# Optimization experiments

Hardware: AMD Instinct MI355X
Metric: run time of the kernel (lower is better)

Reference implementation:

```python
import jax, jax.numpy as jnp
import numpy as np

B, C, H, W = 8, 16, 64, 64
D, N = 1, 512  # embedding_dim, num_embeddings


def setup_inputs() -> dict:
    key = jax.random.key(0)
    k1, k2 = jax.random.split(key)
    x = jax.random.normal(k1, (B, C, H, W), dtype=jnp.float32)
    weight = jax.random.uniform(k2, (D, N), dtype=jnp.float32)  # torch.rand init
    return {"x": x, "weight": weight}


def reference(x, weight):
    b, c, h, w = x.shape
    # dist: [B,C,H,W,N] via broadcast (D==1), argmin over codebook axis
    dist = (x[..., None] - weight) ** 2
    argmin = jnp.argmin(dist, axis=-1)  # [B,C,H,W] int
    # faithful replication of index_select + view([B,H,W,C]) + permute(0,3,1,2)
    codes = jnp.take(weight.T, argmin.reshape(-1), axis=0)  # [B*C*H*W, 1]
    quantized = codes.reshape(b, h, w, c).transpose(0, 3, 1, 2)  # [B,C,H,W]
    e_latent_loss = jnp.mean((x - jax.lax.stop_gradient(quantized)) ** 2)
    q_latent_loss = jnp.mean((quantized - jax.lax.stop_gradient(x)) ** 2)
    # straight-through estimator
    quantized_st = x + jax.lax.stop_gradient(quantized - x)
    return quantized_st, q_latent_loss, e_latent_loss
```

## Files before the change

kernel.cpp:

```cpp
#include <hip/hip_runtime.h>
#include <hip/hip_bf16.h>


#define E_TOTAL 524288
#define NCODE   512
#define BLOCK   256
#define M       2
#define NBLOCKS_M (E_TOTAL / (BLOCK * M))

#define SKEW(a) ((a) + ((a) >> 5))

__global__ __launch_bounds__(64) void vq_prep_kernel(
    const float* __restrict__ wt, float* __restrict__ sorted) {
  __shared__ float4 lw4[NCODE / 4];
  const int t = threadIdx.x;
  lw4[t] = ((const float4*)wt)[t];
  lw4[t + 64] = ((const float4*)wt)[t + 64];
  __syncthreads();

  const int i = blockIdx.x * 64 + t;
  const float v = ((const float*)lw4)[i];
  int r = 0;
#pragma unroll 8
  for (int j = 0; j < NCODE / 4; ++j) {
    const float4 u = lw4[j];
    const int n0 = 4 * j;
    r += (u.x < v || (u.x == v && (n0 + 0) < i)) ? 1 : 0;
    r += (u.y < v || (u.y == v && (n0 + 1) < i)) ? 1 : 0;
    r += (u.z < v || (u.z == v && (n0 + 2) < i)) ? 1 : 0;
    r += (u.w < v || (u.w == v && (n0 + 3) < i)) ? 1 : 0;
  }
  sorted[r] = v;
}

__global__ __launch_bounds__(BLOCK) void vq_main_kernel(
    const float* __restrict__ x, const float* __restrict__ sorted,
    float* __restrict__ out, double* __restrict__ partial) {
  __shared__ float ls[SKEW(NCODE + 1) + 1];
  __shared__ double lsum[BLOCK / 64];

  const int t = threadIdx.x;
  const int tid = blockIdx.x * BLOCK + t;
  const int o0 = tid * M;
  const int w = o0 & 63;
  const int h = (o0 >> 6) & 63;
  const int c = (o0 >> 12) & 15;
  const int b = o0 >> 16;
  const int ip0 = b * 65536 + h * 1024 + w * 16 + c;

  const float g0 = x[ip0];
  const float g1 = x[ip0 + 16];
  const float2 xo = ((const float2*)x)[tid];

  for (int k = t; k < NCODE; k += BLOCK) ls[SKEW(k + 1)] = sorted[k];
  if (t == 0) ls[SKEW(0)] = -3.0e38f;
  __syncthreads();

  unsigned i0 = 0, i1 = 0;
#pragma unroll
  for (unsigned step = NCODE / 2; step; step >>= 1) {
    const float s0 = ls[SKEW(i0 + step)];
    const float s1 = ls[SKEW(i1 + step)];
    i0 = (s0 <= g0) ? i0 + step : i0;
    i1 = (s1 <= g1) ? i1 + step : i1;
  }
  const float l0 = ls[SKEW(i0)], r0 = ls[SKEW(i0 + 1)];
  const float l1 = ls[SKEW(i1)], r1 = ls[SKEW(i1 + 1)];
  const float dl0 = g0 - l0, dr0 = g0 - r0;
  const float dl1 = g1 - l1, dr1 = g1 - r1;
  const float wq0 = (dl0 * dl0 <= dr0 * dr0) ? l0 : r0;
  const float wq1 = (dl1 * dl1 <= dr1 * dr1) ? l1 : r1;

  ((float2*)out)[tid] = make_float2(wq0, wq1);

  const float d0 = xo.x - wq0;
  const float d1 = xo.y - wq1;
  double ds = (double)d0 * (double)d0 + (double)d1 * (double)d1;

#pragma unroll
  for (int off = 32; off > 0; off >>= 1) ds += __shfl_down(ds, off, 64);
  const int lane = t & 63, wave = t >> 6;
  if (lane == 0) lsum[wave] = ds;
  __syncthreads();
  if (t == 0) {
    double s = 0.0;
#pragma unroll
    for (int i = 0; i < BLOCK / 64; ++i) s += lsum[i];
    partial[blockIdx.x] = s;
  }
}

__global__ __launch_bounds__(BLOCK) void vq_reduce_kernel(
    const double* __restrict__ partial, float* __restrict__ out) {
  __shared__ double lsum[BLOCK / 64];
  const int t = threadIdx.x;
  double s = 0.0;
  for (int k = t; k < NBLOCKS_M; k += BLOCK) s += partial[k];
#pragma unroll
  for (int off = 32; off > 0; off >>= 1) s += __shfl_down(s, off, 64);
  const int lane = t & 63, wave = t >> 6;
  if (lane == 0) lsum[wave] = s;
  __syncthreads();
  if (t == 0) {
    double tot = 0.0;
#pragma unroll
    for (int i = 0; i < BLOCK / 64; ++i) tot += lsum[i];
    const float m = (float)(tot / (double)E_TOTAL);
    out[E_TOTAL] = m;
    out[E_TOTAL + 1] = m;
  }
}

extern "C" void kernel_launch(void* const* d_in, const int* in_sizes, int n_in,
                              void* d_out, int out_size, void* d_ws, size_t ws_size,
                              hipStream_t stream) {
  const float* x = (const float*)d_in[0];
  const float* wt = (const float*)d_in[1];
  float* out = (float*)d_out;
  float* sorted = (float*)d_ws;
  double* partial = (double*)((char*)d_ws + 4096);

  vq_prep_kernel<<<8, 64, 0, stream>>>(wt, sorted);
  vq_main_kernel<<<NBLOCKS_M, BLOCK, 0, stream>>>(x, sorted, out, partial);
  vq_reduce_kernel<<<1, BLOCK, 0, stream>>>(partial, out);
}
```

Before: 78.37 us.

## Fuse final loss reduction into main kernel via hierarchical atomic counters

Drops the separate single-block reduce kernel. The last block to finish, found through two levels of atomic counters (32 padded group counters plus one global counter), now sums the per-block partials inside the main kernel. The prep kernel zeroes the counters before each run. This saves one kernel launch and its dependency gap, at the cost of threadfences and atomics at the end of every block and a serial tail in the winning block.

```diff
diff --git a/kernel.cpp b/kernel.cpp
--- a/kernel.cpp
+++ b/kernel.cpp
@@ -7,15 +7,23 @@
 #define BLOCK   256
 #define M       2
 #define NBLOCKS_M (E_TOTAL / (BLOCK * M))
+#define GROUPS  32
+#define GSIZE   (NBLOCKS_M / GROUPS)
 
 #define SKEW(a) ((a) + ((a) >> 5))
 
+
 __global__ __launch_bounds__(64) void vq_prep_kernel(
-    const float* __restrict__ wt, float* __restrict__ sorted) {
+    const float* __restrict__ wt, float* __restrict__ sorted,
+    unsigned* __restrict__ cnt1, unsigned* __restrict__ cnt2) {
   __shared__ float4 lw4[NCODE / 4];
   const int t = threadIdx.x;
   lw4[t] = ((const float4*)wt)[t];
   lw4[t + 64] = ((const float4*)wt)[t + 64];
+  if (blockIdx.x == 0) {
+    if (t < GROUPS) cnt1[t * 32] = 0u;
+    if (t == 32) *cnt2 = 0u;
+  }
   __syncthreads();
 
   const int i = blockIdx.x * 64 + t;
@@ -35,9 +43,11 @@
 
 __global__ __launch_bounds__(BLOCK) void vq_main_kernel(
     const float* __restrict__ x, const float* __restrict__ sorted,
-    float* __restrict__ out, double* __restrict__ partial) {
+    float* __restrict__ out, double* __restrict__ partial,
+    unsigned* __restrict__ cnt1, unsigned* __restrict__ cnt2) {
   __shared__ float ls[SKEW(NCODE + 1) + 1];
   __shared__ double lsum[BLOCK / 64];
+  __shared__ int winner;
 
   const int t = threadIdx.x;
   const int tid = blockIdx.x * BLOCK + t;
@@ -87,27 +97,32 @@
 #pragma unroll
     for (int i = 0; i < BLOCK / 64; ++i) s += lsum[i];
     partial[blockIdx.x] = s;
+    __threadfence();
+    winner = 0;
+    const unsigned old = atomicAdd(&cnt1[(blockIdx.x >> 5) * 32], 1u);
+    if (old == GSIZE - 1) {
+      __threadfence();
+      const unsigned old2 = atomicAdd(cnt2, 1u);
+      if (old2 == GROUPS - 1) winner = 1;
+    }
   }
-}
-
-__global__ __launch_bounds__(BLOCK) void vq_reduce_kernel(
-    const double* __restrict__ partial, float* __restrict__ out) {
-  __shared__ double lsum[BLOCK / 64];
-  const int t = threadIdx.x;
-  double s = 0.0;
-  for (int k = t; k < NBLOCKS_M; k += BLOCK) s += partial[k];
+  __syncthreads();
+  if (winner) {
+    __threadfence();
+    double s2 = 0.0;
+    for (int k = t; k < NBLOCKS_M; k += BLOCK) s2 += partial[k];
 #pragma unroll
-  for (int off = 32; off > 0; off >>= 1) s += __shfl_down(s, off, 64);
-  const int lane = t & 63, wave = t >> 6;
-  if (lane == 0) lsum[wave] = s;
-  __syncthreads();
-  if (t == 0) {
-    double tot = 0.0;
+    for (int off = 32; off > 0; off >>= 1) s2 += __shfl_down(s2, off, 64);
+    if (lane == 0) lsum[wave] = s2;
+    __syncthreads();
+    if (t == 0) {
+      double tot = 0.0;
 #pragma unroll
-    for (int i = 0; i < BLOCK / 64; ++i) tot += lsum[i];
-    const float m = (float)(tot / (double)E_TOTAL);
-    out[E_TOTAL] = m;
-    out[E_TOTAL + 1] = m;
+      for (int i = 0; i < BLOCK / 64; ++i) tot += lsum[i];
+      const float m = (float)(tot / (double)E_TOTAL);
+      out[E_TOTAL] = m;
+      out[E_TOTAL + 1] = m;
+    }
   }
 }
 
@@ -119,8 +134,10 @@
   float* out = (float*)d_out;
   float* sorted = (float*)d_ws;
   double* partial = (double*)((char*)d_ws + 4096);
+  unsigned* cnt1 = (unsigned*)((char*)d_ws + 16384);
+  unsigned* cnt2 = (unsigned*)((char*)d_ws + 20480);
 
-  vq_prep_kernel<<<8, 64, 0, stream>>>(wt, sorted);
-  vq_main_kernel<<<NBLOCKS_M, BLOCK, 0, stream>>>(x, sorted, out, partial);
-  vq_reduce_kernel<<<1, BLOCK, 0, stream>>>(partial, out);
+  vq_prep_kernel<<<8, 64, 0, stream>>>(wt, sorted, cnt1, cnt2);
+  vq_main_kernel<<<NBLOCKS_M, BLOCK, 0, stream>>>(x, sorted, out, partial,
+                                                  cnt1, cnt2);
 }
```

After: 96.45 us. 23.1% more time.
